# Performance work log

Hardware: AMD Instinct MI355X
Metric: run time of the kernel (lower is better)

Reference implementation:

```python
import jax, jax.numpy as jnp
import numpy as np

NUM_GRAPHS = 16
EPS = 1e-5
HEADS = 4


def setup_inputs() -> dict:
    key = jax.random.key(0)
    ks = jax.random.split(key, 20)
    N, E, D = 100000, 1600000, 128
    s = 1.0 / np.sqrt(D)
    inp = {
        'x': jax.random.normal(ks[0], (N, 6), jnp.float32),
        'edge_index': jax.random.randint(ks[1], (2, E), 0, N),
        'norm': jax.random.uniform(ks[2], (E,), jnp.float32),
        'batch': jnp.sort(jax.random.randint(ks[3], (N,), 0, NUM_GRAPHS)),
        'num_layers': 5,
        'enc_w': jax.random.normal(ks[4], (D, 6), jnp.float32) * 0.4,
        'gru_wih': jax.random.normal(ks[5], (3 * D, D), jnp.float32) * s,
        'gru_whh': jax.random.normal(ks[6], (3 * D, D), jnp.float32) * s,
        'gru_bih': jax.random.normal(ks[7], (3 * D,), jnp.float32) * 0.01,
        'gru_bhh': jax.random.normal(ks[8], (3 * D,), jnp.float32) * 0.01,
        'gn_w': jnp.ones((D,), jnp.float32),
        'gn_b': jnp.zeros((D,), jnp.float32),
        'gn_ms': jnp.ones((D,), jnp.float32),
        'in_proj_w': jax.random.normal(ks[9], (3 * D, D), jnp.float32) * s,
        'in_proj_b': jnp.zeros((3 * D,), jnp.float32),
        'out_w': jax.random.normal(ks[10], (D, D), jnp.float32) * s,
        'out_b': jnp.zeros((D,), jnp.float32),
        'dec1_w': jax.random.normal(ks[11], (D // 2, D), jnp.float32) * s,
        'dec2_w': jax.random.normal(ks[12], (1, D // 2), jnp.float32) * s,
    }
    return inp


def _graph_norm(h, batch, gn_w, gn_b, gn_ms):
    # PyG GraphNorm: per-graph mean/var with learnable mean_scale
    cnt = jax.ops.segment_sum(jnp.ones((h.shape[0], 1), h.dtype), batch,
                              num_segments=NUM_GRAPHS)  # [G,1]
    mean = jax.ops.segment_sum(h, batch, num_segments=NUM_GRAPHS) / cnt  # [G,D]
    out = h - mean[batch] * gn_ms
    var = jax.ops.segment_sum(out * out, batch, num_segments=NUM_GRAPHS) / cnt
    return out * jax.lax.rsqrt(var[batch] + EPS) * gn_w + gn_b


def _gru_cell(xin, h, wih, whh, bih, bhh):
    D = h.shape[-1]
    gi = xin @ wih.T + bih  # [N,3D]
    gh = h @ whh.T + bhh
    r = jax.nn.sigmoid(gi[:, :D] + gh[:, :D])
    z = jax.nn.sigmoid(gi[:, D:2 * D] + gh[:, D:2 * D])
    n = jnp.tanh(gi[:, 2 * D:] + r * gh[:, 2 * D:])
    return (1.0 - z) * n + z * h


def reference(x, edge_index, norm, batch, num_layers, enc_w, gru_wih, gru_whh,
              gru_bih, gru_bhh, gn_w, gn_b, gn_ms, in_proj_w, in_proj_b,
              out_w, out_b, dec1_w, dec2_w):
    N = x.shape[0]
    D = enc_w.shape[0]
    src, dst = edge_index[0], edge_index[1]

    h = jax.nn.leaky_relu(x @ enc_w.T)  # dropout is identity in eval
    h_list = [h]
    prev = h
    for _ in range(num_layers):
        # scatter-add neighborhood aggregation: sum_j norm_e * h[src_e] at dst_e
        agg = jax.ops.segment_sum(norm[:, None] * prev[src], dst, num_segments=N)
        h = _gru_cell(agg, prev, gru_wih, gru_whh, gru_bih, gru_bhh) + prev
        h = _graph_norm(h, batch, gn_w, gn_b, gn_ms)
        h_list.append(h)
        prev = h

    hs = jnp.stack(h_list, axis=1)  # [N, S, D], S = num_layers+1
    S = hs.shape[1]
    dh = D // HEADS
    qkv = hs @ in_proj_w.T + in_proj_b  # [N,S,3D]
    q, k, v = jnp.split(qkv, 3, axis=-1)
    q = q.reshape(N, S, HEADS, dh)
    k = k.reshape(N, S, HEADS, dh)
    v = v.reshape(N, S, HEADS, dh)
    scores = jnp.einsum('nshd,nthd->nhst', q, k) / np.sqrt(dh)
    attn = jax.nn.softmax(scores, axis=-1)  # attn dropout off in eval
    ctx = jnp.einsum('nhst,nthd->nshd', attn, v).reshape(N, S, D)
    h_final = ctx @ out_w.T + out_b + hs
    z = jnp.sum(h_final, axis=1)  # [N,D]

    y = jax.nn.leaky_relu(z @ dec1_w.T)
    y = y @ dec2_w.T  # [N,1]
    return y.reshape(-1)
```

## Files before the change

kernel.cpp:

```cpp
#include <hip/hip_runtime.h>

#define NL 5
#define SS 6
#define DD 128
#define GG 16
#define GNB 32
#define APB 8
#define SCB 1024

typedef __bf16 bf16x8 __attribute__((ext_vector_type(8)));
typedef float f32x4 __attribute__((ext_vector_type(4)));
typedef unsigned short ushort_t;

__device__ __forceinline__ float bf2f(unsigned int u) {
  union { unsigned int i; float f; } c; c.i = u << 16; return c.f;
}
__device__ __forceinline__ ushort_t f2bf(float f) {
  union { __bf16 b; ushort_t u; } c; c.b = (__bf16)f;
  return c.u;
}

__global__ void k_deg(const int* __restrict__ ei, int E, int* __restrict__ deg) {
  int e = blockIdx.x * 256 + threadIdx.x;
  if (e < E) atomicAdd(&deg[ei[E + e]], 1);
}

__global__ void k_scan1(const int* __restrict__ deg, int* __restrict__ off,
                        int* __restrict__ bsum, int N) {
  __shared__ int tmp[SCB];
  int t = threadIdx.x, i = blockIdx.x * SCB + t;
  int v = (i < N) ? deg[i] : 0;
  tmp[t] = v; __syncthreads();
  for (int o = 1; o < SCB; o <<= 1) {
    int a = (t >= o) ? tmp[t - o] : 0;
    __syncthreads(); tmp[t] += a; __syncthreads();
  }
  if (i < N) off[i] = tmp[t] - v;
  if (t == SCB - 1) bsum[blockIdx.x] = tmp[t];
}

__global__ void k_scan2(int* __restrict__ bsum, int nb) {
  __shared__ int tmp[SCB];
  int t = threadIdx.x;
  int v = (t < nb) ? bsum[t] : 0;
  tmp[t] = v; __syncthreads();
  for (int o = 1; o < SCB; o <<= 1) {
    int a = (t >= o) ? tmp[t - o] : 0;
    __syncthreads(); tmp[t] += a; __syncthreads();
  }
  if (t < nb) bsum[t] = tmp[t] - v;
}

__global__ void k_scan3(int* __restrict__ off, const int* __restrict__ bsum, int N, int E) {
  int i = blockIdx.x * 256 + threadIdx.x;
  if (i < N) off[i] += bsum[i >> 10];
  else if (i == N) off[N] = E;
}

__global__ void k_copy(const int* __restrict__ a, int* __restrict__ b, int n) {
  int i = blockIdx.x * 256 + threadIdx.x;
  if (i < n) b[i] = a[i];
}

__global__ void k_fill(const int* __restrict__ ei, const float* __restrict__ norm, int E,
                       int* __restrict__ cur, int* __restrict__ csrs, float* __restrict__ csrn) {
  int e = blockIdx.x * 256 + threadIdx.x;
  if (e >= E) return;
  int s = ei[e], d = ei[E + e];
  int p = atomicAdd(&cur[d], 1);
  csrs[p] = s;
  csrn[p] = norm[e];
}

__global__ void k_bend(const int* __restrict__ batch, int N, int* __restrict__ endp) {
  int i = blockIdx.x * 256 + threadIdx.x;
  if (i >= N) return;
  int b = batch[i];
  if (i == N - 1 || batch[i + 1] != b) endp[b] = i + 1;
}

__global__ void k_cnt(const int* __restrict__ endp, int* __restrict__ cnt) {
  if (threadIdx.x == 0 && blockIdx.x == 0) {
    int prev = 0;
    for (int g = 0; g < GG; ++g) {
      int e = endp[g];
      if (e > prev) { cnt[g] = e - prev; prev = e; }
      else cnt[g] = 0;
    }
  }
}

__global__ void k_wconv(const float* __restrict__ wih, const float* __restrict__ whh,
                        const float* __restrict__ ipw, const float* __restrict__ ow,
                        const float* __restrict__ d1,
                        ushort_t* __restrict__ WB, ushort_t* __restrict__ WI,
                        ushort_t* __restrict__ WO, ushort_t* __restrict__ WD1) {
  int o = blockIdx.x * 256 + threadIdx.x;
  int seg, idx;
  if (o < 98304) { seg = 0; idx = o; }
  else if (o < 98304 + 49152) { seg = 1; idx = o - 98304; }
  else if (o < 98304 + 49152 + 16384) { seg = 2; idx = o - 98304 - 49152; }
  else if (o < 98304 + 49152 + 16384 + 8192) { seg = 3; idx = o - 98304 - 49152 - 16384; }
  else return;
  int j = idx & 7, l = (idx >> 3) & 63, ks = (idx >> 9) & 3, ctg = idx >> 11;
  int row = ctg * 16 + (l & 15);
  int col = ks * 32 + ((l >> 4) << 3) + j;
  float v;
  if (seg == 0) { v = (row < 384) ? wih[row * 128 + col] : whh[(row - 384) * 128 + col]; WB[idx] = f2bf(v); }
  else if (seg == 1) { WI[idx] = f2bf(ipw[row * 128 + col]); }
  else if (seg == 2) { WO[idx] = f2bf(ow[row * 128 + col]); }
  else { WD1[idx] = f2bf(d1[row * 128 + col]); }
}

__global__ void k_encode(const float* __restrict__ x, const float* __restrict__ ew,
                         ushort_t* __restrict__ HS, int N) {
  int idx = blockIdx.x * 256 + threadIdx.x;
  if (idx >= N * 64) return;
  int n = idx >> 6, d0 = (idx & 63) << 1;
  float xr[6];
#pragma unroll
  for (int k = 0; k < 6; ++k) xr[k] = x[n * 6 + k];
  float a0 = 0.f, a1 = 0.f;
#pragma unroll
  for (int k = 0; k < 6; ++k) {
    a0 += xr[k] * ew[d0 * 6 + k];
    a1 += xr[k] * ew[(d0 + 1) * 6 + k];
  }
  a0 = a0 > 0.f ? a0 : 0.01f * a0;
  a1 = a1 > 0.f ? a1 : 0.01f * a1;
  unsigned int pk = (unsigned int)f2bf(a0) | ((unsigned int)f2bf(a1) << 16);
  *(unsigned int*)&HS[((size_t)n * SS) * DD + d0] = pk;
}

__global__ __launch_bounds__(256) void k_agg(const ushort_t* __restrict__ HS, int l,
    const int* __restrict__ off, const int* __restrict__ csrs, const float* __restrict__ csrn,
    ushort_t* __restrict__ AGG, float* __restrict__ SUMS, int N) {
  if (blockIdx.x == 0) {
    for (int i = threadIdx.x; i < 2 * GG * DD; i += 256) SUMS[i] = 0.f;
  }
  int n = blockIdx.x * 4 + (threadIdx.x >> 6);
  if (n >= N) return;
  int lane = threadIdx.x & 63;
  int p0 = off[n], p1 = off[n + 1];
  float ax = 0.f, ay = 0.f;
  const ushort_t* base = HS + l * DD + lane * 2;
  int p = p0;
  for (; p + 16 <= p1; p += 16) {
    int s[16]; float w[16]; unsigned int u[16];
#pragma unroll
    for (int q = 0; q < 16; ++q) { s[q] = csrs[p + q]; w[q] = csrn[p + q]; }
#pragma unroll
    for (int q = 0; q < 16; ++q) u[q] = *(const unsigned int*)(base + (size_t)s[q] * (SS * DD));
#pragma unroll
    for (int q = 0; q < 16; ++q) {
      ax += w[q] * bf2f(u[q] & 0xffffu);
      ay += w[q] * bf2f(u[q] >> 16);
    }
  }
  for (; p + 4 <= p1; p += 4) {
    int s[4]; float w[4]; unsigned int u[4];
#pragma unroll
    for (int q = 0; q < 4; ++q) { s[q] = csrs[p + q]; w[q] = csrn[p + q]; }
#pragma unroll
    for (int q = 0; q < 4; ++q) u[q] = *(const unsigned int*)(base + (size_t)s[q] * (SS * DD));
#pragma unroll
    for (int q = 0; q < 4; ++q) {
      ax += w[q] * bf2f(u[q] & 0xffffu);
      ay += w[q] * bf2f(u[q] >> 16);
    }
  }
  for (; p < p1; ++p) {
    int s0 = csrs[p];
    float w0 = csrn[p];
    unsigned int u0 = *(const unsigned int*)(base + (size_t)s0 * (SS * DD));
    ax += w0 * bf2f(u0 & 0xffffu);
    ay += w0 * bf2f(u0 >> 16);
  }
  unsigned int pk = (unsigned int)f2bf(ax) | ((unsigned int)f2bf(ay) << 16);
  *(unsigned int*)&AGG[(size_t)n * DD + lane * 2] = pk;
}

__global__ __launch_bounds__(256) void k_gru(const ushort_t* __restrict__ AGG,
    ushort_t* __restrict__ HS, int l,
    const ushort_t* __restrict__ WB,
    const float* __restrict__ bih, const float* __restrict__ bhh,
    const int* __restrict__ batch, float* __restrict__ SUMS, int N) {
  __shared__ ushort_t axh[2][GNB][136];
  __shared__ ushort_t hout[GNB][136];
  float* SUMSQ = SUMS + GG * DD;
  int t = threadIdx.x;
  int nb = blockIdx.x * GNB;
#pragma unroll
  for (int it = 0; it < 2; ++it) {
    int n = (t >> 4) + it * 16, k8 = (t & 15) << 3;
    int gn = nb + n;
    uint4 xv = make_uint4(0, 0, 0, 0), hv = xv;
    if (gn < N) {
      xv = *(const uint4*)&AGG[(size_t)gn * DD + k8];
      hv = *(const uint4*)&HS[((size_t)gn * SS + l) * DD + k8];
    }
    *(uint4*)&axh[0][n][k8] = xv;
    *(uint4*)&axh[1][n][k8] = hv;
  }
  __syncthreads();
  int w = t >> 6, lane = t & 63, r = lane & 15, kl = lane >> 4;
  int nlast = min(nb + GNB, N) - 1;
  int bu = batch[nb];
  bool uni = (batch[nlast] == bu);
#pragma unroll
  for (int ct2 = 0; ct2 < 2; ++ct2) {
    f32x4 acc[6][2];
#pragma unroll
    for (int src = 0; src < 2; ++src) {
      bf16x8 af[2][4];
#pragma unroll
      for (int rt = 0; rt < 2; ++rt)
#pragma unroll
        for (int ks = 0; ks < 4; ++ks)
          af[rt][ks] = *(const bf16x8*)&axh[src][rt * 16 + r][ks * 32 + kl * 8];
#pragma unroll
      for (int q3 = 0; q3 < 3; ++q3) {
        int q = src * 3 + q3;
        int ctg = q * 8 + w * 2 + ct2;
        f32x4 a0 = {0.f, 0.f, 0.f, 0.f}, a1 = a0;
#pragma unroll
        for (int ks = 0; ks < 4; ++ks) {
          bf16x8 bf = *(const bf16x8*)&WB[(((size_t)ctg * 4 + ks) << 9) + (lane << 3)];
          a0 = __builtin_amdgcn_mfma_f32_16x16x32_bf16(af[0][ks], bf, a0, 0, 0, 0);
          a1 = __builtin_amdgcn_mfma_f32_16x16x32_bf16(af[1][ks], bf, a1, 0, 0, 0);
        }
        acc[q][0] = a0;
        acc[q][1] = a1;
      }
    }
    int d = w * 32 + ct2 * 16 + r;
    float br = bih[d], bz = bih[128 + d], bn2 = bih[256 + d];
    float cr = bhh[d], cz = bhh[128 + d], cn2 = bhh[256 + d];
    float loc = 0.f, locq = 0.f;
#pragma unroll
    for (int rt = 0; rt < 2; ++rt) {
#pragma unroll
      for (int i = 0; i < 4; ++i) {
        int n = rt * 16 + kl * 4 + i;
        int gn = nb + n;
        if (gn < N) {
          float gir = acc[0][rt][i] + br, giz = acc[1][rt][i] + bz, gin = acc[2][rt][i] + bn2;
          float ghr = acc[3][rt][i] + cr, ghz = acc[4][rt][i] + cz, ghn = acc[5][rt][i] + cn2;
          float rr = 1.f / (1.f + __expf(-(gir + ghr)));
          float zz = 1.f / (1.f + __expf(-(giz + ghz)));
          float nn = tanhf(gin + rr * ghn);
          float prev = bf2f(axh[1][n][d]);
          float hp = (1.f - zz) * nn + zz * prev + prev;
          hout[n][d] = f2bf(hp);
          if (uni) { loc += hp; locq += hp * hp; }
          else {
            atomicAdd(&SUMS[batch[gn] * DD + d], hp);
            atomicAdd(&SUMSQ[batch[gn] * DD + d], hp * hp);
          }
        }
      }
    }
    if (uni) {
      loc += __shfl_xor(loc, 16);
      loc += __shfl_xor(loc, 32);
      locq += __shfl_xor(locq, 16);
      locq += __shfl_xor(locq, 32);
      if (kl == 0) {
        atomicAdd(&SUMS[bu * DD + d], loc);
        atomicAdd(&SUMSQ[bu * DD + d], locq);
      }
    }
  }
  __syncthreads();
#pragma unroll
  for (int it = 0; it < 2; ++it) {
    int n = (t >> 4) + it * 16, k8 = (t & 15) << 3;
    int gn = nb + n;
    if (gn < N)
      *(uint4*)&HS[((size_t)gn * SS + l + 1) * DD + k8] = *(const uint4*)&hout[n][k8];
  }
}

__global__ void k_gn(ushort_t* __restrict__ HS, int slot,
    const float* __restrict__ SUMS, const int* __restrict__ CNT,
    const int* __restrict__ batch, const float* __restrict__ gms,
    const float* __restrict__ gw, const float* __restrict__ gb, int N) {
  const float* SUMSQ = SUMS + GG * DD;
  int idx = blockIdx.x * 256 + threadIdx.x;
  if (idx >= N * 16) return;
  int n = idx >> 4, d0 = (idx & 15) << 3;
  int b = batch[n];
  float inv = 1.f / (float)CNT[b];
  size_t o = ((size_t)n * SS + slot) * DD + d0;
  uint4 hv = *(const uint4*)&HS[o];
  unsigned int uu[4] = {hv.x, hv.y, hv.z, hv.w};
  unsigned int out[4];
#pragma unroll
  for (int j = 0; j < 4; ++j) {
    ushort_t res[2];
#pragma unroll
    for (int k = 0; k < 2; ++k) {
      int d = d0 + j * 2 + k;
      float mean = SUMS[b * DD + d] * inv;
      float m = mean * gms[d];
      float var = SUMSQ[b * DD + d] * inv - 2.f * m * mean + m * m;
      float h = bf2f(k ? (uu[j] >> 16) : (uu[j] & 0xffffu));
      float v = (h - m) * rsqrtf(var + 1e-5f) * gw[d] + gb[d];
      res[k] = f2bf(v);
    }
    out[j] = (unsigned int)res[0] | ((unsigned int)res[1] << 16);
  }
  uint4 ov = make_uint4(out[0], out[1], out[2], out[3]);
  *(uint4*)&HS[o] = ov;
}

__global__ __launch_bounds__(256) void k_attn(const ushort_t* __restrict__ HS,
    const ushort_t* __restrict__ WI, const float* __restrict__ ipb,
    const ushort_t* __restrict__ WO, const float* __restrict__ ob,
    const ushort_t* __restrict__ WD1, const float* __restrict__ d2,
    float* __restrict__ y, int N) {
  __shared__ ushort_t hsb[64][136];
  __shared__ ushort_t qk[4][2][16][40];
  __shared__ ushort_t ctxb[16][136];
  __shared__ float hss[8][132];
  ushort_t (*zb)[136] = (ushort_t(*)[136])&qk[0][0][0][0];
  float* ypart = &hss[0][0];
  int t = threadIdx.x;
  int nb = blockIdx.x * APB;
  for (int idx = t; idx < 64 * 16; idx += 256) {
    int row = idx >> 4, k8 = (idx & 15) << 3;
    int n = row >> 3, s = row & 7;
    uint4 v = make_uint4(0, 0, 0, 0);
    if (s < 6 && nb + n < N) v = *(const uint4*)&HS[((size_t)(nb + n) * SS + s) * DD + k8];
    *(uint4*)&hsb[row][k8] = v;
  }
  __syncthreads();
  {
    int n = t >> 5, d0 = (t & 31) << 2;
    float a0 = 0.f, a1 = 0.f, a2 = 0.f, a3 = 0.f;
#pragma unroll
    for (int s = 0; s < 6; ++s) {
      const ushort_t* rp = &hsb[n * 8 + s][d0];
      unsigned int u0 = *(const unsigned int*)rp;
      unsigned int u1 = *(const unsigned int*)(rp + 2);
      a0 += bf2f(u0 & 0xffffu); a1 += bf2f(u0 >> 16);
      a2 += bf2f(u1 & 0xffffu); a3 += bf2f(u1 >> 16);
    }
    hss[n][d0] = a0; hss[n][d0 + 1] = a1; hss[n][d0 + 2] = a2; hss[n][d0 + 3] = a3;
  }
  int w = t >> 6, lane = t & 63, r = lane & 15, kl = lane >> 4;
  const float sc32 = 0.17677669529663687f;
#pragma unroll
  for (int rt = 0; rt < 4; ++rt) {
    bf16x8 af[4];
#pragma unroll
    for (int ks = 0; ks < 4; ++ks)
      af[ks] = *(const bf16x8*)&hsb[rt * 16 + r][ks * 32 + kl * 8];
    float vreg[2][4];
#pragma unroll
    for (int ct2 = 0; ct2 < 2; ++ct2) {
      int cq = 2 * w + ct2, ck = 8 + 2 * w + ct2, cv = 16 + 2 * w + ct2;
      f32x4 aq = {0.f, 0.f, 0.f, 0.f}, ak = aq, av = aq;
#pragma unroll
      for (int ks = 0; ks < 4; ++ks) {
        bf16x8 bq = *(const bf16x8*)&WI[(((size_t)cq * 4 + ks) << 9) + (lane << 3)];
        bf16x8 bk = *(const bf16x8*)&WI[(((size_t)ck * 4 + ks) << 9) + (lane << 3)];
        bf16x8 bv = *(const bf16x8*)&WI[(((size_t)cv * 4 + ks) << 9) + (lane << 3)];
        aq = __builtin_amdgcn_mfma_f32_16x16x32_bf16(af[ks], bq, aq, 0, 0, 0);
        ak = __builtin_amdgcn_mfma_f32_16x16x32_bf16(af[ks], bk, ak, 0, 0, 0);
        av = __builtin_amdgcn_mfma_f32_16x16x32_bf16(af[ks], bv, av, 0, 0, 0);
      }
      int colh = ct2 * 16 + r;
      float bq = ipb[w * 32 + colh];
      float bk = ipb[128 + w * 32 + colh];
#pragma unroll
      for (int i = 0; i < 4; ++i) {
        qk[w][0][kl * 4 + i][colh] = f2bf((aq[i] + bq) * sc32);
        qk[w][1][kl * 4 + i][colh] = f2bf(ak[i] + bk);
        vreg[ct2][i] = av[i];
      }
    }
    bf16x8 aq = *(const bf16x8*)&qk[w][0][r][kl * 8];
    bf16x8 bk = *(const bf16x8*)&qk[w][1][r][kl * 8];
    f32x4 s4 = {0.f, 0.f, 0.f, 0.f};
    s4 = __builtin_amdgcn_mfma_f32_16x16x32_bf16(aq, bk, s4, 0, 0, 0);
    bool tval = (r & 7) < 6;
    float mx = -1e30f;
    float sc[4]; bool val[4];
#pragma unroll
    for (int i = 0; i < 4; ++i) {
      int ss = 4 * kl + i;
      val[i] = tval && (((ss ^ r) & 8) == 0) && ((ss & 7) < 6);
      sc[i] = s4[i];
      if (val[i]) mx = fmaxf(mx, sc[i]);
    }
#pragma unroll
    for (int m = 1; m <= 4; m <<= 1) mx = fmaxf(mx, __shfl_xor(mx, m));
    float e[4], sum[4];
#pragma unroll
    for (int i = 0; i < 4; ++i) {
      e[i] = val[i] ? __expf(sc[i] - mx) : 0.f;
      sum[i] = e[i];
#pragma unroll
      for (int m = 1; m <= 4; m <<= 1) sum[i] += __shfl_xor(sum[i], m);
    }
    float awp = 0.f;
#pragma unroll
    for (int i = 0; i < 4; ++i) {
      int ss = 4 * kl + i;
      float attn = (((ss & 7) < 6) && sum[i] > 0.f) ? e[i] / sum[i] : 0.f;
      awp += attn;
    }
    awp += __shfl_xor(awp, 16);
    awp += __shfl_xor(awp, 32);
    float awv[4];
#pragma unroll
    for (int i = 0; i < 4; ++i) {
      int tt = 4 * (kl & 1) + i;
      awv[i] = __shfl(awp, (kl >> 1) * 8 + (tt < 8 ? tt : 0));
    }
    int nodei = 2 * rt + (kl >> 1);
#pragma unroll
    for (int ct2 = 0; ct2 < 2; ++ct2) {
      float acc = 0.f;
#pragma unroll
      for (int i = 0; i < 4; ++i) {
        int tt = 4 * (kl & 1) + i;
        if (tt < 6) acc += awv[i] * vreg[ct2][i];
      }
      acc += __shfl_xor(acc, 16);
      int dcol = w * 32 + ct2 * 16 + r;
      if ((kl & 1) == 0) ctxb[nodei][dcol] = f2bf(acc + 6.f * ipb[256 + dcol]);
    }
  }
  __syncthreads();
  {
    bf16x8 ac[4];
#pragma unroll
    for (int ks = 0; ks < 4; ++ks)
      ac[ks] = *(const bf16x8*)&ctxb[r][ks * 32 + kl * 8];
#pragma unroll
    for (int c2 = 0; c2 < 2; ++c2) {
      int ctg = 2 * w + c2;
      f32x4 a = {0.f, 0.f, 0.f, 0.f};
#pragma unroll
      for (int ks = 0; ks < 4; ++ks) {
        bf16x8 bf = *(const bf16x8*)&WO[(((size_t)ctg * 4 + ks) << 9) + (lane << 3)];
        a = __builtin_amdgcn_mfma_f32_16x16x32_bf16(ac[ks], bf, a, 0, 0, 0);
      }
      int col = ctg * 16 + r;
      float obv = 6.f * ob[col];
#pragma unroll
      for (int i = 0; i < 4; ++i) {
        int row = kl * 4 + i;
        float zv = (row < 8) ? (a[i] + obv + hss[row][col]) : 0.f;
        zb[row][col] = f2bf(zv);
      }
    }
  }
  __syncthreads();
  {
    bf16x8 az[4];
#pragma unroll
    for (int ks = 0; ks < 4; ++ks)
      az[ks] = *(const bf16x8*)&zb[r][ks * 32 + kl * 8];
    f32x4 a = {0.f, 0.f, 0.f, 0.f};
#pragma unroll
    for (int ks = 0; ks < 4; ++ks) {
      bf16x8 bf = *(const bf16x8*)&WD1[(((size_t)w * 4 + ks) << 9) + (lane << 3)];
      a = __builtin_amdgcn_mfma_f32_16x16x32_bf16(az[ks], bf, a, 0, 0, 0);
    }
    float dv = d2[w * 16 + r];
    float part[4];
#pragma unroll
    for (int i = 0; i < 4; ++i) {
      float u = a[i];
      u = u > 0.f ? u : 0.01f * u;
      part[i] = u * dv;
    }
#pragma unroll
    for (int m = 1; m <= 8; m <<= 1) {
#pragma unroll
      for (int i = 0; i < 4; ++i) part[i] += __shfl_xor(part[i], m);
    }
    if (r == 0) {
#pragma unroll
      for (int i = 0; i < 4; ++i) {
        int row = kl * 4 + i;
        if (row < 8) ypart[w * 8 + row] = part[i];
      }
    }
  }
  __syncthreads();
  if (t < 8) {
    float v = ypart[t] + ypart[8 + t] + ypart[16 + t] + ypart[24 + t];
    if (nb + t < N) y[nb + t] = v;
  }
}

extern "C" void kernel_launch(void* const* d_in, const int* in_sizes, int n_in,
                              void* d_out, int out_size, void* d_ws, size_t ws_size,
                              hipStream_t stream) {
  const float* x    = (const float*)d_in[0];
  const int*   ei   = (const int*)d_in[1];
  const float* norm = (const float*)d_in[2];
  const int*   batch= (const int*)d_in[3];
  const float* enc_w= (const float*)d_in[5];
  const float* wih  = (const float*)d_in[6];
  const float* whh  = (const float*)d_in[7];
  const float* bih  = (const float*)d_in[8];
  const float* bhh  = (const float*)d_in[9];
  const float* gw   = (const float*)d_in[10];
  const float* gb   = (const float*)d_in[11];
  const float* gms  = (const float*)d_in[12];
  const float* ipw  = (const float*)d_in[13];
  const float* ipb  = (const float*)d_in[14];
  const float* ow   = (const float*)d_in[15];
  const float* ob   = (const float*)d_in[16];
  const float* d1   = (const float*)d_in[17];
  const float* d2   = (const float*)d_in[18];
  float* y = (float*)d_out;
  int N = in_sizes[3];
  int E = in_sizes[2];

  char* p = (char*)d_ws;
  ushort_t* HS  = (ushort_t*)p;  p += (size_t)N * SS * DD * 2;
  ushort_t* AGG = (ushort_t*)p;  p += (size_t)N * DD * 2;
  ushort_t* WB  = (ushort_t*)p;  p += (size_t)98304 * 2;
  ushort_t* WI  = (ushort_t*)p;  p += (size_t)49152 * 2;
  ushort_t* WO  = (ushort_t*)p;  p += (size_t)16384 * 2;
  ushort_t* WD1 = (ushort_t*)p;  p += (size_t)8192 * 2;
  float* SUMS = (float*)p;       p += GG * DD * 4;
  float* SUMSQ= (float*)p;       p += GG * DD * 4;   (void)SUMSQ;
  int*   CNT  = (int*)p;         p += GG * 4;
  int*   ENDP = (int*)p;         p += GG * 4;
  int*   BSUM = (int*)p;         p += SCB * 4;
  int*   OFF  = (int*)p;         p += ((size_t)N + 1) * 4;
  int*   CUR  = (int*)p;         p += (size_t)N * 4;
  int*   CSRS = (int*)p;         p += (size_t)E * 4;
  float* CSRN = (float*)p;

  int nchunk = (N + SCB - 1) / SCB;

  hipMemsetAsync(CUR, 0, (size_t)N * 4, stream);
  hipMemsetAsync(CNT, 0, 2 * GG * 4, stream);
  k_deg<<<(E + 255) / 256, 256, 0, stream>>>(ei, E, CUR);
  k_scan1<<<nchunk, SCB, 0, stream>>>(CUR, OFF, BSUM, N);
  k_scan2<<<1, SCB, 0, stream>>>(BSUM, nchunk);
  k_scan3<<<(N + 256) / 256, 256, 0, stream>>>(OFF, BSUM, N, E);
  k_copy<<<(N + 255) / 256, 256, 0, stream>>>(OFF, CUR, N);
  k_fill<<<(E + 255) / 256, 256, 0, stream>>>(ei, norm, E, CUR, CSRS, CSRN);
  k_bend<<<(N + 255) / 256, 256, 0, stream>>>(batch, N, ENDP);
  k_cnt<<<1, 64, 0, stream>>>(ENDP, CNT);
  k_wconv<<<672, 256, 0, stream>>>(wih, whh, ipw, ow, d1, WB, WI, WO, WD1);
  k_encode<<<(N * 64 + 255) / 256, 256, 0, stream>>>(x, enc_w, HS, N);

  for (int l = 0; l < NL; ++l) {
    k_agg<<<(N + 3) / 4, 256, 0, stream>>>(HS, l, OFF, CSRS, CSRN, AGG, SUMS, N);
    k_gru<<<(N + GNB - 1) / GNB, 256, 0, stream>>>(AGG, HS, l, WB, bih, bhh, batch, SUMS, N);
    k_gn<<<(N * 16 + 255) / 256, 256, 0, stream>>>(HS, l + 1, SUMS, CNT, batch, gms, gw, gb, N);
  }
  k_attn<<<(N + APB - 1) / APB, 256, 0, stream>>>(HS, WI, ipb, WO, ob, WD1, d2, y, N);
}
```

Baseline: 1.276 ms.

## Widen aggregation gathers, fuse scan copy, hoist V weights in attention

```diff
diff --git a/kernel.cpp b/kernel.cpp
--- a/kernel.cpp
+++ b/kernel.cpp
@@ -51,15 +51,14 @@
   if (t < nb) bsum[t] = tmp[t] - v;
 }
 
-__global__ void k_scan3(int* __restrict__ off, const int* __restrict__ bsum, int N, int E) {
+__global__ void k_scan3(int* __restrict__ off, int* __restrict__ cur,
+                        const int* __restrict__ bsum, int N, int E) {
   int i = blockIdx.x * 256 + threadIdx.x;
-  if (i < N) off[i] += bsum[i >> 10];
-  else if (i == N) off[N] = E;
-}
-
-__global__ void k_copy(const int* __restrict__ a, int* __restrict__ b, int n) {
-  int i = blockIdx.x * 256 + threadIdx.x;
-  if (i < n) b[i] = a[i];
+  if (i < N) {
+    int v = off[i] + bsum[i >> 10];
+    off[i] = v;
+    cur[i] = v;
+  } else if (i == N) off[N] = E;
 }
 
 __global__ void k_fill(const int* __restrict__ ei, const float* __restrict__ norm, int E,
@@ -138,46 +137,54 @@
   if (blockIdx.x == 0) {
     for (int i = threadIdx.x; i < 2 * GG * DD; i += 256) SUMS[i] = 0.f;
   }
-  int n = blockIdx.x * 4 + (threadIdx.x >> 6);
+  int n = blockIdx.x * 8 + (threadIdx.x >> 5);
   if (n >= N) return;
-  int lane = threadIdx.x & 63;
+  int lane = threadIdx.x & 31;
   int p0 = off[n], p1 = off[n + 1];
-  float ax = 0.f, ay = 0.f;
-  const ushort_t* base = HS + l * DD + lane * 2;
+  float a0 = 0.f, a1 = 0.f, a2 = 0.f, a3 = 0.f;
+  const ushort_t* base = HS + l * DD + lane * 4;
   int p = p0;
   for (; p + 16 <= p1; p += 16) {
-    int s[16]; float w[16]; unsigned int u[16];
+    int s[16]; float w[16]; uint2 u[16];
 #pragma unroll
     for (int q = 0; q < 16; ++q) { s[q] = csrs[p + q]; w[q] = csrn[p + q]; }
 #pragma unroll
-    for (int q = 0; q < 16; ++q) u[q] = *(const unsigned int*)(base + (size_t)s[q] * (SS * DD));
+    for (int q = 0; q < 16; ++q) u[q] = *(const uint2*)(base + (size_t)s[q] * (SS * DD));
 #pragma unroll
     for (int q = 0; q < 16; ++q) {
-      ax += w[q] * bf2f(u[q] & 0xffffu);
-      ay += w[q] * bf2f(u[q] >> 16);
+      a0 += w[q] * bf2f(u[q].x & 0xffffu);
+      a1 += w[q] * bf2f(u[q].x >> 16);
+      a2 += w[q] * bf2f(u[q].y & 0xffffu);
+      a3 += w[q] * bf2f(u[q].y >> 16);
     }
   }
   for (; p + 4 <= p1; p += 4) {
-    int s[4]; float w[4]; unsigned int u[4];
+    int s[4]; float w[4]; uint2 u[4];
 #pragma unroll
     for (int q = 0; q < 4; ++q) { s[q] = csrs[p + q]; w[q] = csrn[p + q]; }
 #pragma unroll
-    for (int q = 0; q < 4; ++q) u[q] = *(const unsigned int*)(base + (size_t)s[q] * (SS * DD));
+    for (int q = 0; q < 4; ++q) u[q] = *(const uint2*)(base + (size_t)s[q] * (SS * DD));
 #pragma unroll
     for (int q = 0; q < 4; ++q) {
-      ax += w[q] * bf2f(u[q] & 0xffffu);
-      ay += w[q] * bf2f(u[q] >> 16);
+      a0 += w[q] * bf2f(u[q].x & 0xffffu);
+      a1 += w[q] * bf2f(u[q].x >> 16);
+      a2 += w[q] * bf2f(u[q].y & 0xffffu);
+      a3 += w[q] * bf2f(u[q].y >> 16);
     }
   }
   for (; p < p1; ++p) {
     int s0 = csrs[p];
     float w0 = csrn[p];
-    unsigned int u0 = *(const unsigned int*)(base + (size_t)s0 * (SS * DD));
-    ax += w0 * bf2f(u0 & 0xffffu);
-    ay += w0 * bf2f(u0 >> 16);
-  }
-  unsigned int pk = (unsigned int)f2bf(ax) | ((unsigned int)f2bf(ay) << 16);
-  *(unsigned int*)&AGG[(size_t)n * DD + lane * 2] = pk;
+    uint2 u0 = *(const uint2*)(base + (size_t)s0 * (SS * DD));
+    a0 += w0 * bf2f(u0.x & 0xffffu);
+    a1 += w0 * bf2f(u0.x >> 16);
+    a2 += w0 * bf2f(u0.y & 0xffffu);
+    a3 += w0 * bf2f(u0.y >> 16);
+  }
+  uint2 pk;
+  pk.x = (unsigned int)f2bf(a0) | ((unsigned int)f2bf(a1) << 16);
+  pk.y = (unsigned int)f2bf(a2) | ((unsigned int)f2bf(a3) << 16);
+  *(uint2*)&AGG[(size_t)n * DD + lane * 4] = pk;
 }
 
 __global__ __launch_bounds__(256) void k_gru(const ushort_t* __restrict__ AGG,
@@ -314,7 +321,7 @@
   *(uint4*)&HS[o] = ov;
 }
 
-__global__ __launch_bounds__(256) void k_attn(const ushort_t* __restrict__ HS,
+__global__ __launch_bounds__(256, 4) void k_attn(const ushort_t* __restrict__ HS,
     const ushort_t* __restrict__ WI, const float* __restrict__ ipb,
     const ushort_t* __restrict__ WO, const float* __restrict__ ob,
     const ushort_t* __restrict__ WD1, const float* __restrict__ d2,
@@ -350,6 +357,12 @@
   }
   int w = t >> 6, lane = t & 63, r = lane & 15, kl = lane >> 4;
   const float sc32 = 0.17677669529663687f;
+  bf16x8 bvh[2][4];
+#pragma unroll
+  for (int ct2 = 0; ct2 < 2; ++ct2)
+#pragma unroll
+    for (int ks = 0; ks < 4; ++ks)
+      bvh[ct2][ks] = *(const bf16x8*)&WI[(((size_t)(16 + 2 * w + ct2) * 4 + ks) << 9) + (lane << 3)];
 #pragma unroll
   for (int rt = 0; rt < 4; ++rt) {
     bf16x8 af[4];
@@ -359,16 +372,15 @@
     float vreg[2][4];
 #pragma unroll
     for (int ct2 = 0; ct2 < 2; ++ct2) {
-      int cq = 2 * w + ct2, ck = 8 + 2 * w + ct2, cv = 16 + 2 * w + ct2;
+      int cq = 2 * w + ct2, ck = 8 + 2 * w + ct2;
       f32x4 aq = {0.f, 0.f, 0.f, 0.f}, ak = aq, av = aq;
 #pragma unroll
       for (int ks = 0; ks < 4; ++ks) {
         bf16x8 bq = *(const bf16x8*)&WI[(((size_t)cq * 4 + ks) << 9) + (lane << 3)];
         bf16x8 bk = *(const bf16x8*)&WI[(((size_t)ck * 4 + ks) << 9) + (lane << 3)];
-        bf16x8 bv = *(const bf16x8*)&WI[(((size_t)cv * 4 + ks) << 9) + (lane << 3)];
         aq = __builtin_amdgcn_mfma_f32_16x16x32_bf16(af[ks], bq, aq, 0, 0, 0);
         ak = __builtin_amdgcn_mfma_f32_16x16x32_bf16(af[ks], bk, ak, 0, 0, 0);
-        av = __builtin_amdgcn_mfma_f32_16x16x32_bf16(af[ks], bv, av, 0, 0, 0);
+        av = __builtin_amdgcn_mfma_f32_16x16x32_bf16(af[ks], bvh[ct2][ks], av, 0, 0, 0);
       }
       int colh = ct2 * 16 + r;
       float bq = ipb[w * 32 + colh];
@@ -547,8 +559,7 @@
   k_deg<<<(E + 255) / 256, 256, 0, stream>>>(ei, E, CUR);
   k_scan1<<<nchunk, SCB, 0, stream>>>(CUR, OFF, BSUM, N);
   k_scan2<<<1, SCB, 0, stream>>>(BSUM, nchunk);
-  k_scan3<<<(N + 256) / 256, 256, 0, stream>>>(OFF, BSUM, N, E);
-  k_copy<<<(N + 255) / 256, 256, 0, stream>>>(OFF, CUR, N);
+  k_scan3<<<(N + 256) / 256, 256, 0, stream>>>(OFF, CUR, BSUM, N, E);
   k_fill<<<(E + 255) / 256, 256, 0, stream>>>(ei, norm, E, CUR, CSRS, CSRN);
   k_bend<<<(N + 255) / 256, 256, 0, stream>>>(batch, N, ENDP);
   k_cnt<<<1, 64, 0, stream>>>(ENDP, CNT);
@@ -556,7 +567,7 @@
   k_encode<<<(N * 64 + 255) / 256, 256, 0, stream>>>(x, enc_w, HS, N);
 
   for (int l = 0; l < NL; ++l) {
-    k_agg<<<(N + 3) / 4, 256, 0, stream>>>(HS, l, OFF, CSRS, CSRN, AGG, SUMS, N);
+    k_agg<<<(N + 7) / 8, 256, 0, stream>>>(HS, l, OFF, CSRS, CSRN, AGG, SUMS, N);
     k_gru<<<(N + GNB - 1) / GNB, 256, 0, stream>>>(AGG, HS, l, WB, bih, bhh, batch, SUMS, N);
     k_gn<<<(N * 16 + 255) / 256, 256, 0, stream>>>(HS, l + 1, SUMS, CNT, batch, gms, gw, gb, N);
   }
```

Result: slower. 1.312 ms (+2.8%).
